# Optimization experiments

Measured on AMD Instinct MI355X. Metric: run time of the kernel, lower is better.

## Reference

```python
import jax, jax.numpy as jnp
import numpy as np

N = 256   # units (waveguides)
L = 256   # num_layers (rectangular mesh: L == N)
B = 16384 # batch
TWO_PI = 2.0 * np.pi


def _perm_indices():
    # Rectangular-mesh column permutations: alternate +/-1 circular shifts so
    # successive columns couple (0,1),(2,3),... then (1,2),(3,4),...; final
    # permutation undoes the net shift (perm_layers has L+1 entries).
    ar = np.arange(N)
    shifts = [0] + [(1 if l % 2 == 1 else -1) for l in range(1, L)]
    perms = [(ar + s) % N for s in shifts]
    perms.append((ar - sum(shifts)) % N)
    return np.asarray(perms, dtype=np.int32)  # (L+1, N)


def setup_inputs() -> dict:
    key = jax.random.key(0)
    ks = jax.random.split(key, 5)
    x_re = jax.random.normal(ks[0], (B, N), jnp.float32)
    x_im = jax.random.normal(ks[1], (B, N), jnp.float32)
    theta = jax.random.uniform(ks[2], (L, N // 2), jnp.float32) * TWO_PI
    phi = jax.random.uniform(ks[3], (L, N // 2), jnp.float32) * TWO_PI
    gamma = jax.random.uniform(ks[4], (N,), jnp.float32) * TWO_PI
    perm_idx = jnp.asarray(_perm_indices())
    pp = np.arange(N).reshape(-1, 2)[:, ::-1].reshape(-1)  # [1,0,3,2,...]
    pairwise_perm_idx = jnp.asarray(pp, dtype=jnp.int32)
    return dict(x_re=x_re, x_im=x_im, theta=theta, phi=phi, gamma=gamma,
                perm_idx=perm_idx, pairwise_perm_idx=pairwise_perm_idx)


def _mesh_diag_offdiag(theta, phi):
    # Bloch basis, differential internal arrangement: +theta/2 on top port
    # (even waveguide), -theta/2 on bottom port (odd waveguide).
    t = theta.T  # (N/2, L)
    internal = jnp.stack([t * 0.5, -t * 0.5], axis=1).reshape(N, L)
    # single-mode external arrangement: phi on top port, 0 on bottom.
    external = jnp.stack([phi.T, jnp.zeros_like(phi.T)], axis=1).reshape(N, L)
    ipsl = jnp.exp(1j * internal)   # (N, L) complex64
    epsl = jnp.exp(1j * external)
    up = lambda a: jnp.roll(a, -1, axis=0)   # roll_tensor(x, up=True)
    dn = lambda a: jnp.roll(a, 1, axis=0)    # roll_tensor(x)
    e = jnp.float32(0.5)  # ideal 50:50 splitters -> all mzi_error_tensors = 0.5
    # hadamard = False branch of Mesh.mesh_layers
    s11 = e * ipsl - e * up(ipsl)
    s22 = dn(-e * ipsl + e * up(ipsl))
    s12 = 1j * dn(e * ipsl + e * up(ipsl))
    s21 = 1j * (e * ipsl + e * up(ipsl))
    diag = epsl * (s11 + s22) * 0.5
    off = dn(epsl) * (s21 + s12) * 0.5
    return diag.T, off.T  # (L, N)


def reference(x_re, x_im, theta, phi, gamma, perm_idx, pairwise_perm_idx):
    diag, off = _mesh_diag_offdiag(theta, phi)
    # include_diagonal_phases: input phase screen exp(i*gamma)
    x = (x_re + 1j * x_im) * jnp.exp(1j * gamma)[None, :]

    def step(x, lay):
        perm, d, o = lay
        x = jnp.take(x, perm, axis=-1)                              # PermutationLayer
        x = x * d + jnp.take(x * o, pairwise_perm_idx, axis=-1)     # MZI couple
        return x, None

    x, _ = jax.lax.scan(step, x, (perm_idx[:L], diag, off))
    x = jnp.take(x, perm_idx[L], axis=-1)  # right_perm of final layer
    return jnp.stack([jnp.real(x), jnp.imag(x)])  # (2, B, N) float32
```

## Files before the change

kernel.cpp:

```cpp
#include <hip/hip_runtime.h>
#include <math.h>

#define NN 256
#define LL 256
#define BB 16384

typedef __attribute__((ext_vector_type(8))) short short8;
typedef __attribute__((ext_vector_type(4))) float f32x4;


__global__ void tab_kernel(const float* __restrict__ theta,
                           const float* __restrict__ phi,
                           double2* __restrict__ ipt,
                           double2* __restrict__ ept) {
    int idx = blockIdx.x * blockDim.x + threadIdx.x;
    if (idx >= LL * 128) return;
    double s, c;
    sincos((double)theta[idx] * 0.5, &s, &c);
    ipt[idx] = make_double2(c, s);
    sincos((double)phi[idx], &s, &c);
    ept[idx] = make_double2(c, s);
}

__global__ void coef_kernel(const double2* __restrict__ ipt,
                            const double2* __restrict__ ept,
                            const float* __restrict__ gamma,
                            float4* __restrict__ coef) {
    int idx = blockIdx.x * blockDim.x + threadIdx.x;
    if (idx >= LL * NN) return;
    int l = idx >> 8, j = idx & 255;
    int u = l & 1;
    int n = (j - u) & 255;
    int m = n ^ 1;
    const double2* ip = ipt + l * 128;
    const double2* ep = ept + l * 128;

    auto ipsl = [&](int k, double& re, double& im) {
        k &= 255;
        double2 v = ip[k >> 1];
        re = v.x; im = (k & 1) ? -v.y : v.y;
    };
    double inr, ini, ipr, ipi, imr, imi;
    ipsl(n, inr, ini); ipsl(n + 1, ipr, ipi); ipsl(n - 1, imr, imi);
    double enr = 1.0, eni = 0.0;
    if (!(n & 1)) { double2 v = ep[n >> 1]; enr = v.x; eni = v.y; }
    double dr = 2.0 * inr - ipr - imr;
    double di = 2.0 * ini - ipi - imi;
    double Dre = 0.25 * (enr * dr - eni * di);
    double Dim = 0.25 * (enr * di + eni * dr);
    ipsl(m, inr, ini); ipsl(m + 1, ipr, ipi); ipsl(m - 1, imr, imi);
    int mm = (m - 1) & 255;
    double emr = 1.0, emi = 0.0;
    if (!(mm & 1)) { double2 v = ep[mm >> 1]; emr = v.x; emi = v.y; }
    double orv = 2.0 * inr + ipr + imr;
    double oiv = 2.0 * ini + ipi + imi;
    double tre = emr * orv - emi * oiv;
    double tim = emr * oiv + emi * orv;
    double Ore = -0.25 * tim;
    double Oim =  0.25 * tre;

    if (l == 0) {
        double s, c;
        sincos((double)gamma[j], &s, &c);
        double a2 = Dre * c - Dim * s, b2 = Dre * s + Dim * c;
        Dre = a2; Dim = b2;
        sincos((double)gamma[j ^ 1], &s, &c);
        a2 = Ore * c - Oim * s; b2 = Ore * s + Oim * c;
        Ore = a2; Oim = b2;
    }
    coef[l * 256 + (j & 7) * 32 + (j >> 3)] =
        make_float4((float)Dre, (float)Dim, (float)Ore, (float)Oim);
}

__device__ __forceinline__ float2 mzi(float2 cD, float2 cO, float2 y, float2 p) {
    float2 t;
    asm("v_pk_mul_f32 %0, %1, %2 op_sel:[1,1] op_sel_hi:[1,0] neg_lo:[1,0]"
        : "=v"(t) : "v"(cO), "v"(p));
    asm("v_pk_fma_f32 %0, %1, %2, %0 op_sel:[0,0,0] op_sel_hi:[0,1,1]"
        : "+v"(t) : "v"(cO), "v"(p));
    asm("v_pk_fma_f32 %0, %1, %2, %0 op_sel:[1,1,0] op_sel_hi:[1,0,1] neg_lo:[1,0,0]"
        : "+v"(t) : "v"(cD), "v"(y));
    asm("v_pk_fma_f32 %0, %1, %2, %0 op_sel:[0,0,0] op_sel_hi:[0,1,1]"
        : "+v"(t) : "v"(cD), "v"(y));
    return t;
}
__device__ __forceinline__ float2 D_(float4 c) { return make_float2(c.x, c.y); }
__device__ __forceinline__ float2 O_(float4 c) { return make_float2(c.z, c.w); }

__global__ __launch_bounds__(256) void prop_kernel(const float4* __restrict__ coef,
                                                   float2* __restrict__ PA,
                                                   float2* __restrict__ PB) {
    const int lane = threadIdx.x & 63;
    const int wave = threadIdx.x >> 6;
    const int l32  = lane & 31;
    const int half = lane >> 5;
    const int gid  = blockIdx.x * 4 + wave;
    const int mhalf = gid >> 6;
    const int c4   = (gid & 63) * 4;
    const int l0   = mhalf ? 128 : 0;
    const int idxL4 = (((lane & 32) | ((lane - 1) & 31))) << 2;
    const int idxR4 = (((lane & 32) | ((lane + 1) & 31))) << 2;

    float2 y[2][8];
#pragma unroll
    for (int s2 = 0; s2 < 2; ++s2) {
        int row = c4 + 2 * s2 + half;
#pragma unroll
        for (int j = 0; j < 8; ++j)
            y[s2][j] = make_float2((8 * l32 + j == row) ? 1.f : 0.f, 0.f);
    }

    const float4* cp = coef + l32;
    auto loadl = [&](int l, float4& c0, float4& c1, float4& c2, float4& c3,
                            float4& c4_, float4& c5, float4& c6, float4& c7) {
        const float4* p = cp + l * 256;
        c0 = p[0 * 32]; c1 = p[1 * 32]; c2 = p[2 * 32]; c3 = p[3 * 32];
        c4_ = p[4 * 32]; c5 = p[5 * 32]; c6 = p[6 * 32]; c7 = p[7 * 32];
    };

    float4 a0, a1, a2, a3, a4, a5, a6, a7;
    float4 b0, b1, b2, b3, b4, b5, b6, b7;
    loadl(l0, a0, a1, a2, a3, a4, a5, a6, a7);

#pragma unroll 1
    for (int it = 0; it < 64; ++it) {
        loadl(l0 + 2 * it + 1, b0, b1, b2, b3, b4, b5, b6, b7);
#pragma unroll
        for (int s2 = 0; s2 < 2; ++s2) {
            float2 t0 = y[s2][0], t1 = y[s2][1], t2 = y[s2][2], t3 = y[s2][3];
            float2 t4 = y[s2][4], t5 = y[s2][5], t6 = y[s2][6], t7 = y[s2][7];
            y[s2][0] = mzi(D_(a0), O_(a0), t0, t1);
            y[s2][1] = mzi(D_(a1), O_(a1), t1, t0);
            y[s2][2] = mzi(D_(a2), O_(a2), t2, t3);
            y[s2][3] = mzi(D_(a3), O_(a3), t3, t2);
            y[s2][4] = mzi(D_(a4), O_(a4), t4, t5);
            y[s2][5] = mzi(D_(a5), O_(a5), t5, t4);
            y[s2][6] = mzi(D_(a6), O_(a6), t6, t7);
            y[s2][7] = mzi(D_(a7), O_(a7), t7, t6);
        }
        if (it < 63) loadl(l0 + 2 * it + 2, a0, a1, a2, a3, a4, a5, a6, a7);
#pragma unroll
        for (int s2 = 0; s2 < 2; ++s2) {
            float2 t0 = y[s2][0], t1 = y[s2][1], t2 = y[s2][2], t3 = y[s2][3];
            float2 t4 = y[s2][4], t5 = y[s2][5], t6 = y[s2][6], t7 = y[s2][7];
            float2 plo, phi2;
            plo.x  = __int_as_float(__builtin_amdgcn_ds_bpermute(idxL4, __float_as_int(t7.x)));
            plo.y  = __int_as_float(__builtin_amdgcn_ds_bpermute(idxL4, __float_as_int(t7.y)));
            phi2.x = __int_as_float(__builtin_amdgcn_ds_bpermute(idxR4, __float_as_int(t0.x)));
            phi2.y = __int_as_float(__builtin_amdgcn_ds_bpermute(idxR4, __float_as_int(t0.y)));
            y[s2][1] = mzi(D_(b1), O_(b1), t1, t2);
            y[s2][2] = mzi(D_(b2), O_(b2), t2, t1);
            y[s2][3] = mzi(D_(b3), O_(b3), t3, t4);
            y[s2][4] = mzi(D_(b4), O_(b4), t4, t3);
            y[s2][5] = mzi(D_(b5), O_(b5), t5, t6);
            y[s2][6] = mzi(D_(b6), O_(b6), t6, t5);
            y[s2][0] = mzi(D_(b0), O_(b0), t0, plo);
            y[s2][7] = mzi(D_(b7), O_(b7), t7, phi2);
        }
    }

    float2* P = mhalf ? PB : PA;
#pragma unroll
    for (int s2 = 0; s2 < 2; ++s2) {
        int row = c4 + 2 * s2 + half;
#pragma unroll
        for (int j = 0; j < 8; ++j)
            P[row * 256 + 8 * l32 + j] = y[s2][j];
    }
}

__device__ __forceinline__ unsigned short bf16rne(float f) {
    unsigned int u2 = __float_as_uint(f);
    unsigned int r = (u2 + 0x7FFFu + ((u2 >> 16) & 1u)) >> 16;
    return (unsigned short)r;
}
__device__ __forceinline__ float bf16f(unsigned short h) {
    return __uint_as_float(((unsigned int)h) << 16);
}
__device__ __forceinline__ void split3(float v, unsigned short& h0,
                                       unsigned short& h1, unsigned short& h2) {
    h0 = bf16rne(v);        float r1 = v - bf16f(h0);
    h1 = bf16rne(r1);       float r2 = r1 - bf16f(h1);
    h2 = bf16rne(r2);
}

__global__ __launch_bounds__(256) void combineW_kernel(const float2* __restrict__ PA,
                                                       const float2* __restrict__ PB,
                                                       unsigned short* __restrict__ Wt) {
    int i = blockIdx.x, j = threadIdx.x;
    float accr = 0.f, acci = 0.f;
#pragma unroll 8
    for (int k = 0; k < 256; ++k) {
        float2 a = PA[i * 256 + k];
        float2 b = PB[k * 256 + j];
        accr += a.x * b.x - a.y * b.y;
        acci += a.x * b.y + a.y * b.x;
    }
    unsigned short r0, r1, r2, i0, i1, i2, n0, n1, n2;
    split3(accr, r0, r1, r2);
    split3(acci, i0, i1, i2);
    split3(-acci, n0, n1, n2);
    unsigned short* W0 = Wt;
    unsigned short* W1 = Wt + 262144;
    unsigned short* W2 = Wt + 524288;
    W0[j * 512 + i] = r0;           W1[j * 512 + i] = r1;           W2[j * 512 + i] = r2;
    W0[(j + 256) * 512 + i] = i0;   W1[(j + 256) * 512 + i] = i1;   W2[(j + 256) * 512 + i] = i2;
    W0[j * 512 + i + 256] = n0;     W1[j * 512 + i + 256] = n1;     W2[j * 512 + i + 256] = n2;
    W0[(j + 256) * 512 + i + 256] = r0;
    W1[(j + 256) * 512 + i + 256] = r1;
    W2[(j + 256) * 512 + i + 256] = r2;
}

__global__ __launch_bounds__(256, 2) void gemm_kernel(
        const float* __restrict__ x_re, const float* __restrict__ x_im,
        const unsigned short* __restrict__ Wt, float* __restrict__ out) {
    __shared__ unsigned short XL[3][128][42];
    __shared__ unsigned short WL[3][128][42];

    const int t    = threadIdx.x;
    const int lane = t & 63;
    const int wave = t >> 6;
    const int wm   = wave >> 1, wn = wave & 1;
    const int Lb = (blockIdx.x & 7) * 64 + (blockIdx.x >> 3);
    const int mt = Lb >> 2, nt = Lb & 3;
    const int m0 = mt * 128, n0 = nt * 128;
    const int lr = lane & 15, lg = lane >> 4;

    float4 xv[4];
    uint4  wv[6];
    const int F   = t;
    const int Un  = t;

    auto load_tiles = [&](int ks) {
        const int k0 = ks * 32;
        const float* xsrc = (k0 < 256) ? x_re : x_im;
        const int kcol = k0 & 255;
#pragma unroll
        for (int r = 0; r < 4; ++r) {
            int Fi = r * 256 + F;
            int row = Fi >> 3, g = Fi & 7;
            xv[r] = ((const float4*)xsrc)[(m0 + row) * 64 + (kcol >> 2) + g];
        }
#pragma unroll
        for (int r = 0; r < 6; ++r) {
            int U = r * 256 + Un;
            int p = U >> 9, rem = U & 511;
            int n = rem >> 2, ku = (rem & 3) * 8;
            wv[r] = ((const uint4*)Wt)[p * 32768 + (n0 + n) * 64 + ((k0 + ku) >> 3)];
        }
    };
    auto write_tiles = [&]() {
#pragma unroll
        for (int r = 0; r < 4; ++r) {
            int Fi = r * 256 + F;
            int row = Fi >> 3, g = Fi & 7;
            float4 v = xv[r];
            unsigned short h0[4], h1[4], h2[4];
            split3(v.x, h0[0], h1[0], h2[0]);
            split3(v.y, h0[1], h1[1], h2[1]);
            split3(v.z, h0[2], h1[2], h2[2]);
            split3(v.w, h0[3], h1[3], h2[3]);
            *(ushort4*)&XL[0][row][g * 4] = make_ushort4(h0[0], h0[1], h0[2], h0[3]);
            *(ushort4*)&XL[1][row][g * 4] = make_ushort4(h1[0], h1[1], h1[2], h1[3]);
            *(ushort4*)&XL[2][row][g * 4] = make_ushort4(h2[0], h2[1], h2[2], h2[3]);
        }
#pragma unroll
        for (int r = 0; r < 6; ++r) {
            int U = r * 256 + Un;
            int p = U >> 9, rem = U & 511;
            int n = rem >> 2, ku = (rem & 3) * 8;
            *(uint4*)&WL[p][n][ku] = wv[r];
        }
    };

    f32x4 acc[4][4];
#pragma unroll
    for (int a = 0; a < 4; ++a)
#pragma unroll
        for (int b = 0; b < 4; ++b) acc[a][b] = (f32x4)0.f;

    load_tiles(0);
    write_tiles();
    __syncthreads();

#pragma unroll 1
    for (int ks = 0; ks < 16; ++ks) {
        if (ks < 15) load_tiles(ks + 1);

        short8 bfr[3][4];
#pragma unroll
        for (int p = 0; p < 3; ++p)
#pragma unroll
            for (int ni = 0; ni < 4; ++ni)
                bfr[p][ni] = *(const short8*)&WL[p][wn * 64 + ni * 16 + lr][lg * 8];
#pragma unroll
        for (int i = 0; i < 3; ++i) {
            short8 af[4];
#pragma unroll
            for (int mi = 0; mi < 4; ++mi)
                af[mi] = *(const short8*)&XL[i][wm * 64 + mi * 16 + lr][lg * 8];
#pragma unroll
            for (int jj = 0; jj < 3; ++jj) {
                if (i + jj > 2) continue;
#pragma unroll
                for (int mi = 0; mi < 4; ++mi)
#pragma unroll
                    for (int ni = 0; ni < 4; ++ni)
                        acc[mi][ni] = __builtin_amdgcn_mfma_f32_16x16x32_bf16(
                            af[mi], bfr[jj][ni], acc[mi][ni], 0, 0, 0);
            }
        }
        __syncthreads();
        if (ks < 15) write_tiles();
        __syncthreads();
    }

#pragma unroll
    for (int mi = 0; mi < 4; ++mi) {
#pragma unroll
        for (int ni = 0; ni < 4; ++ni) {
            int nglob = n0 + wn * 64 + ni * 16 + lr;
            float* dst = (nglob < 256)
                       ? out + (size_t)nglob
                       : out + (size_t)BB * 256 + (nglob - 256);
#pragma unroll
            for (int e = 0; e < 4; ++e) {
                int m = m0 + wm * 64 + mi * 16 + lg * 4 + e;
                dst[(size_t)m * 256] = acc[mi][ni][e];
            }
        }
    }
}

extern "C" void kernel_launch(void* const* d_in, const int* in_sizes, int n_in,
                              void* d_out, int out_size, void* d_ws, size_t ws_size,
                              hipStream_t stream) {
    const float* x_re  = (const float*)d_in[0];
    const float* x_im  = (const float*)d_in[1];
    const float* theta = (const float*)d_in[2];
    const float* phi   = (const float*)d_in[3];
    const float* gamma = (const float*)d_in[4];

    char* ws = (char*)d_ws;
    float4* coef        = (float4*)ws;
    float2* PA          = (float2*)(ws + (1 << 20));
    float2* PB          = (float2*)(ws + (1 << 20) + (512 << 10));
    unsigned short* Wt  = (unsigned short*)(ws + (2 << 20));
    double2* ipt        = (double2*)(ws + (3 << 20) + (512 << 10));
    double2* ept        = (double2*)(ws + (4 << 20));

    hipLaunchKernelGGL(tab_kernel, dim3(128), dim3(256), 0, stream,
                       theta, phi, ipt, ept);
    hipLaunchKernelGGL(coef_kernel, dim3(256), dim3(256), 0, stream,
                       ipt, ept, gamma, coef);
    hipLaunchKernelGGL(prop_kernel, dim3(32), dim3(256), 0, stream, coef, PA, PB);
    hipLaunchKernelGGL(combineW_kernel, dim3(256), dim3(256), 0, stream, PA, PB, Wt);
    hipLaunchKernelGGL(gemm_kernel, dim3(512), dim3(256), 0, stream,
                       x_re, x_im, Wt, (float*)d_out);
}
```

Baseline: 238.4 us.

## Fuse trig table into coef kernel and simplify GEMM tile loading

Merges the sincos table kernel into the coefficient kernel, so each block computes its layer's sines and cosines into shared memory and no longer writes and reads a global table. This removes one launch and a global round trip. The GEMM loses its register prefetch of the next K tile: it now loads, writes to LDS, syncs and computes in sequence. It also drops LDS row padding from 42 to 40 and the block-index swizzle. Together these cut register pressure but expose global load latency and may add LDS bank conflicts and worse cache locality.

```diff
diff --git a/kernel.cpp b/kernel.cpp
--- a/kernel.cpp
+++ b/kernel.cpp
@@ -9,41 +9,34 @@
 typedef __attribute__((ext_vector_type(4))) float f32x4;
 
 
-__global__ void tab_kernel(const float* __restrict__ theta,
-                           const float* __restrict__ phi,
-                           double2* __restrict__ ipt,
-                           double2* __restrict__ ept) {
-    int idx = blockIdx.x * blockDim.x + threadIdx.x;
-    if (idx >= LL * 128) return;
-    double s, c;
-    sincos((double)theta[idx] * 0.5, &s, &c);
-    ipt[idx] = make_double2(c, s);
-    sincos((double)phi[idx], &s, &c);
-    ept[idx] = make_double2(c, s);
-}
-
-__global__ void coef_kernel(const double2* __restrict__ ipt,
-                            const double2* __restrict__ ept,
-                            const float* __restrict__ gamma,
-                            float4* __restrict__ coef) {
-    int idx = blockIdx.x * blockDim.x + threadIdx.x;
-    if (idx >= LL * NN) return;
-    int l = idx >> 8, j = idx & 255;
-    int u = l & 1;
-    int n = (j - u) & 255;
-    int m = n ^ 1;
-    const double2* ip = ipt + l * 128;
-    const double2* ep = ept + l * 128;
+__global__ __launch_bounds__(256) void coefF_kernel(const float* __restrict__ theta,
+                                                    const float* __restrict__ phi,
+                                                    const float* __restrict__ gamma,
+                                                    float4* __restrict__ coef) {
+    __shared__ double ipc[128], ips[128], epc[128], eps[128];
+    const int l = blockIdx.x;
+    const int t = threadIdx.x;
+    if (t < 128) {
+        double s, c;
+        sincos((double)theta[l * 128 + t] * 0.5, &s, &c); ipc[t] = c; ips[t] = s;
+        sincos((double)phi[l * 128 + t], &s, &c);         epc[t] = c; eps[t] = s;
+    }
+    __syncthreads();
+
+    const int j = t;
+    const int u = l & 1;
+    const int n = (j - u) & 255;
+    const int m = n ^ 1;
 
     auto ipsl = [&](int k, double& re, double& im) {
         k &= 255;
-        double2 v = ip[k >> 1];
-        re = v.x; im = (k & 1) ? -v.y : v.y;
+        re = ipc[k >> 1];
+        im = (k & 1) ? -ips[k >> 1] : ips[k >> 1];
     };
     double inr, ini, ipr, ipi, imr, imi;
     ipsl(n, inr, ini); ipsl(n + 1, ipr, ipi); ipsl(n - 1, imr, imi);
     double enr = 1.0, eni = 0.0;
-    if (!(n & 1)) { double2 v = ep[n >> 1]; enr = v.x; eni = v.y; }
+    if (!(n & 1)) { enr = epc[n >> 1]; eni = eps[n >> 1]; }
     double dr = 2.0 * inr - ipr - imr;
     double di = 2.0 * ini - ipi - imi;
     double Dre = 0.25 * (enr * dr - eni * di);
@@ -51,7 +44,7 @@
     ipsl(m, inr, ini); ipsl(m + 1, ipr, ipi); ipsl(m - 1, imr, imi);
     int mm = (m - 1) & 255;
     double emr = 1.0, emi = 0.0;
-    if (!(mm & 1)) { double2 v = ep[mm >> 1]; emr = v.x; emi = v.y; }
+    if (!(mm & 1)) { emr = epc[mm >> 1]; emi = eps[mm >> 1]; }
     double orv = 2.0 * inr + ipr + imr;
     double oiv = 2.0 * ini + ipi + imi;
     double tre = emr * orv - emi * oiv;
@@ -214,47 +207,33 @@
 __global__ __launch_bounds__(256, 2) void gemm_kernel(
         const float* __restrict__ x_re, const float* __restrict__ x_im,
         const unsigned short* __restrict__ Wt, float* __restrict__ out) {
-    __shared__ unsigned short XL[3][128][42];
-    __shared__ unsigned short WL[3][128][42];
+    __shared__ unsigned short XL[3][128][40];
+    __shared__ unsigned short WL[3][128][40];
 
     const int t    = threadIdx.x;
     const int lane = t & 63;
     const int wave = t >> 6;
     const int wm   = wave >> 1, wn = wave & 1;
-    const int Lb = (blockIdx.x & 7) * 64 + (blockIdx.x >> 3);
-    const int mt = Lb >> 2, nt = Lb & 3;
+    const int nt = blockIdx.x & 3, mt = blockIdx.x >> 2;
     const int m0 = mt * 128, n0 = nt * 128;
     const int lr = lane & 15, lg = lane >> 4;
 
-    float4 xv[4];
-    uint4  wv[6];
-    const int F   = t;
-    const int Un  = t;
-
-    auto load_tiles = [&](int ks) {
+    f32x4 acc[4][4];
+#pragma unroll
+    for (int a = 0; a < 4; ++a)
+#pragma unroll
+        for (int b = 0; b < 4; ++b) acc[a][b] = (f32x4)0.f;
+
+#pragma unroll 1
+    for (int ks = 0; ks < 16; ++ks) {
         const int k0 = ks * 32;
         const float* xsrc = (k0 < 256) ? x_re : x_im;
         const int kcol = k0 & 255;
 #pragma unroll
         for (int r = 0; r < 4; ++r) {
-            int Fi = r * 256 + F;
-            int row = Fi >> 3, g = Fi & 7;
-            xv[r] = ((const float4*)xsrc)[(m0 + row) * 64 + (kcol >> 2) + g];
-        }
-#pragma unroll
-        for (int r = 0; r < 6; ++r) {
-            int U = r * 256 + Un;
-            int p = U >> 9, rem = U & 511;
-            int n = rem >> 2, ku = (rem & 3) * 8;
-            wv[r] = ((const uint4*)Wt)[p * 32768 + (n0 + n) * 64 + ((k0 + ku) >> 3)];
-        }
-    };
-    auto write_tiles = [&]() {
-#pragma unroll
-        for (int r = 0; r < 4; ++r) {
-            int Fi = r * 256 + F;
-            int row = Fi >> 3, g = Fi & 7;
-            float4 v = xv[r];
+            int F = r * 256 + t;
+            int row = F >> 3, g = F & 7;
+            float4 v = ((const float4*)xsrc)[(m0 + row) * 64 + (kcol >> 2) + g];
             unsigned short h0[4], h1[4], h2[4];
             split3(v.x, h0[0], h1[0], h2[0]);
             split3(v.y, h0[1], h1[1], h2[1]);
@@ -266,26 +245,13 @@
         }
 #pragma unroll
         for (int r = 0; r < 6; ++r) {
-            int U = r * 256 + Un;
+            int U = r * 256 + t;
             int p = U >> 9, rem = U & 511;
             int n = rem >> 2, ku = (rem & 3) * 8;
-            *(uint4*)&WL[p][n][ku] = wv[r];
-        }
-    };
-
-    f32x4 acc[4][4];
-#pragma unroll
-    for (int a = 0; a < 4; ++a)
-#pragma unroll
-        for (int b = 0; b < 4; ++b) acc[a][b] = (f32x4)0.f;
-
-    load_tiles(0);
-    write_tiles();
-    __syncthreads();
-
-#pragma unroll 1
-    for (int ks = 0; ks < 16; ++ks) {
-        if (ks < 15) load_tiles(ks + 1);
+            uint4 v = ((const uint4*)Wt)[p * 32768 + (n0 + n) * 64 + ((k0 + ku) >> 3)];
+            *(uint4*)&WL[p][n][ku] = v;
+        }
+        __syncthreads();
 
         short8 bfr[3][4];
 #pragma unroll
@@ -293,6 +259,7 @@
 #pragma unroll
             for (int ni = 0; ni < 4; ++ni)
                 bfr[p][ni] = *(const short8*)&WL[p][wn * 64 + ni * 16 + lr][lg * 8];
+
 #pragma unroll
         for (int i = 0; i < 3; ++i) {
             short8 af[4];
@@ -310,8 +277,6 @@
                             af[mi], bfr[jj][ni], acc[mi][ni], 0, 0, 0);
             }
         }
-        __syncthreads();
-        if (ks < 15) write_tiles();
         __syncthreads();
     }
 
@@ -346,13 +311,9 @@
     float2* PA          = (float2*)(ws + (1 << 20));
     float2* PB          = (float2*)(ws + (1 << 20) + (512 << 10));
     unsigned short* Wt  = (unsigned short*)(ws + (2 << 20));
-    double2* ipt        = (double2*)(ws + (3 << 20) + (512 << 10));
-    double2* ept        = (double2*)(ws + (4 << 20));
-
-    hipLaunchKernelGGL(tab_kernel, dim3(128), dim3(256), 0, stream,
-                       theta, phi, ipt, ept);
-    hipLaunchKernelGGL(coef_kernel, dim3(256), dim3(256), 0, stream,
-                       ipt, ept, gamma, coef);
+
+    hipLaunchKernelGGL(coefF_kernel, dim3(256), dim3(256), 0, stream,
+                       theta, phi, gamma, coef);
     hipLaunchKernelGGL(prop_kernel, dim3(32), dim3(256), 0, stream, coef, PA, PB);
     hipLaunchKernelGGL(combineW_kernel, dim3(256), dim3(256), 0, stream, PA, PB, Wt);
     hipLaunchKernelGGL(gemm_kernel, dim3(512), dim3(256), 0, stream,
```

After: 198.8 us. -16.6%, faster.
